# Kernel optimization log

Measured on AMD Instinct MI355X. Metric: run time of the kernel, lower is better.

Reference implementation:

```python
import jax, jax.numpy as jnp
import numpy as np

N_ENT = 100000
N_USR = 1024
E = 400000
D = 128
H = 4
R = 32


def setup_inputs() -> dict:
    key = jax.random.key(0)
    ks = jax.random.split(key, 9)
    a = float(np.sqrt(6.0 / (D + D)))  # xavier_uniform bound for [D, D]
    return {
        "entity_emb": jax.random.normal(ks[0], (N_ENT, D), dtype=jnp.float32),
        "user_emb": jax.random.normal(ks[1], (N_USR, D), dtype=jnp.float32),
        "interact_mat": jnp.zeros((1,), dtype=jnp.float32),  # unused by forward
        "weight": jax.random.normal(ks[2], (R, D), dtype=jnp.float32) * 0.1,
        "qTrans": jax.random.uniform(ks[3], (D, D), minval=-a, maxval=a, dtype=jnp.float32),
        "kTrans": jax.random.uniform(ks[4], (D, D), minval=-a, maxval=a, dtype=jnp.float32),
        "vTrans": jax.random.uniform(ks[5], (D, D), minval=-a, maxval=a, dtype=jnp.float32),
        "edge_index": jax.random.randint(ks[6], (2, E), 0, N_ENT, dtype=jnp.int64)
            if jax.config.jax_enable_x64 else jax.random.randint(ks[6], (2, E), 0, N_ENT, dtype=jnp.int32),
        "edge_type": jax.random.randint(ks[7], (E,), 1, R + 1, dtype=jnp.int32),  # types in [1, R]
        "layer": 0,
    }


def _kglayer(rows, col_embeds, embeds, n_seg, qT, kT, vT):
    # rows: [E] target-node index, col_embeds: [E, D] edge messages
    dh = D // H
    row_embeds = embeds[rows]                              # gather [E, D]
    q = (row_embeds @ qT).reshape(-1, H, dh)
    k = (col_embeds @ kT).reshape(-1, H, dh)
    v = (col_embeds @ vT).reshape(-1, H, dh)
    att = jnp.clip(jnp.einsum("ehd,ehd->eh", q, k), -10.0, 10.0)
    exp_att = jnp.exp(att)                                 # [E, H]
    att_norm = jax.ops.segment_sum(exp_att, rows, num_segments=n_seg)[rows]
    att = exp_att / (att_norm + 1e-8)
    res = (att[..., None] * v).reshape(-1, D)              # [E, D]
    return jax.ops.segment_sum(res, rows, num_segments=n_seg)


def _sim_hrt(head_emb, tail_emb, rel_emb):
    # per-edge scalar attention logit [E, 1]
    tr = jnp.linalg.norm(tail_emb * rel_emb, axis=1, keepdims=True)
    hr = jnp.linalg.norm(head_emb * rel_emb, axis=1, keepdims=True)
    return (hr * tr) ** 2


def reference(entity_emb, user_emb, interact_mat, weight, qTrans, kTrans, vTrans,
              edge_index, edge_type, layer):
    n_entities = entity_emb.shape[0]
    head, tail = edge_index[0], edge_index[1]
    rel = weight[edge_type - 1]                            # [E, D]
    neigh = entity_emb[tail] * rel                         # [E, D]
    kg_emb = _kglayer(head, neigh, entity_emb, n_entities, qTrans, kTrans, vTrans)
    w = _sim_hrt(kg_emb[head], kg_emb[tail], rel)          # [E, 1]
    w = jnp.broadcast_to(w, neigh.shape)                   # expand to [E, D]
    # scatter_softmax over edges sharing the same head (numerically stable)
    m = jax.ops.segment_max(w, head, num_segments=n_entities)[head]
    e = jnp.exp(w - m)
    s = jax.ops.segment_sum(e, head, num_segments=n_entities)[head]
    soft = e / s
    msg = soft * entity_emb[tail]
    return jax.ops.segment_sum(msg, head, num_segments=n_entities)
```

## Files before the change

kernel.cpp:

```cpp
#include <hip/hip_runtime.h>
#include <cstdint>

#define D 128
#define H 4
#define N_ENT 100000
#define N_EDGE 400000
#define R 32

#define SCAN_NB ((N_ENT + 511) / 512)

__global__ void k_hist(const int* __restrict__ head, int* __restrict__ deg) {
  const int e = blockIdx.x * 256 + threadIdx.x;
  if (e < N_EDGE) atomicAdd(&deg[head[e]], 1);
}

__global__ __launch_bounds__(256) void k_scan1(const int* __restrict__ deg,
                                               int* __restrict__ bsum) {
  const int t = threadIdx.x;
  const int i = blockIdx.x * 512 + t * 2;
  int v0 = (i < N_ENT) ? deg[i] : 0;
  int v1 = (i + 1 < N_ENT) ? deg[i + 1] : 0;
  int s = v0 + v1;
#pragma unroll
  for (int k = 1; k < 64; k <<= 1) s += __shfl_xor(s, k);
  __shared__ int ws[4];
  if ((t & 63) == 0) ws[t >> 6] = s;
  __syncthreads();
  if (t == 0) bsum[blockIdx.x] = ws[0] + ws[1] + ws[2] + ws[3];
}

__global__ __launch_bounds__(256) void k_scan2(const int* __restrict__ bsum,
                                               int* __restrict__ bbase,
                                               int* __restrict__ off) {
  __shared__ int sh[256];
  const int t = threadIdx.x;
  const int v = (t < SCAN_NB) ? bsum[t] : 0;
  sh[t] = v;
  __syncthreads();
  for (int d = 1; d < 256; d <<= 1) {
    const int u = (t >= d) ? sh[t - d] : 0;
    __syncthreads();
    sh[t] += u;
    __syncthreads();
  }
  if (t < SCAN_NB) bbase[t] = sh[t] - v;
  if (t == SCAN_NB - 1) off[N_ENT] = sh[t];
}

__global__ __launch_bounds__(256) void k_scan3(const int* __restrict__ deg,
                                               const int* __restrict__ bbase,
                                               int* __restrict__ off,
                                               int* __restrict__ cur) {
  __shared__ int sh[256];
  const int t = threadIdx.x;
  const int i = blockIdx.x * 512 + t * 2;
  const int v0 = (i < N_ENT) ? deg[i] : 0;
  const int v1 = (i + 1 < N_ENT) ? deg[i + 1] : 0;
  const int s = v0 + v1;
  sh[t] = s;
  __syncthreads();
  for (int d = 1; d < 256; d <<= 1) {
    const int u = (t >= d) ? sh[t - d] : 0;
    __syncthreads();
    sh[t] += u;
    __syncthreads();
  }
  const int ex = sh[t] - s + bbase[blockIdx.x];
  if (i < N_ENT) {
    off[i] = ex;
    cur[i] = ex;
  }
  if (i + 1 < N_ENT) {
    off[i + 1] = ex + v0;
    cur[i + 1] = ex + v0;
  }
}

__global__ void k_scatter(const int* __restrict__ head,
                          const int* __restrict__ tail,
                          const int* __restrict__ etype, int* __restrict__ cur,
                          int* __restrict__ tailP, int* __restrict__ etypeP) {
  const int e = blockIdx.x * 256 + threadIdx.x;
  if (e >= N_EDGE) return;
  const int hd = head[e];
  const int pos = atomicAdd(&cur[hd], 1);
  tailP[pos] = tail[e];
  etypeP[pos] = etype[e] - 1;
}

__global__ __launch_bounds__(256) void k_tr(const float* __restrict__ in,
                                            float* __restrict__ out) {
  __shared__ float tile[32][33];
  const int bx = blockIdx.x & 3, by = blockIdx.x >> 2;
  const int c = threadIdx.x & 31;
  const int r0 = (threadIdx.x >> 5) * 4;
#pragma unroll
  for (int i = 0; i < 4; ++i)
    tile[r0 + i][c] = in[(by * 32 + r0 + i) * 128 + bx * 32 + c];
  __syncthreads();
#pragma unroll
  for (int i = 0; i < 4; ++i)
    out[(bx * 32 + r0 + i) * 128 + by * 32 + c] = tile[c][r0 + i];
}

__global__ __launch_bounds__(512) void k_qproj(const float* __restrict__ ent,
                                               const float* __restrict__ qT,
                                               float* __restrict__ Q) {
  __shared__ float sT[D * D];
  __shared__ float rows[D * 128];
  const int t = threadIdx.x;
  const int n0 = blockIdx.x * 128;
#pragma unroll
  for (int s = 0; s < 8; ++s) {
    const int idx = (s * 512 + t) * 4;
    *(float4*)&sT[idx] = *(const float4*)&qT[idx];
  }
  {
    const int g = t & 3;
    const int n = t >> 2;
    const int node = n0 + n;
    if (node < N_ENT) {
      const float* src = ent + (size_t)node * D;
#pragma unroll
      for (int s = 0; s < 8; ++s) {
        const int i = s * 16 + g * 4;
        float4 v = *(const float4*)&src[i];
        rows[(i + 0) * 128 + n] = v.x;
        rows[(i + 1) * 128 + n] = v.y;
        rows[(i + 2) * 128 + n] = v.z;
        rows[(i + 3) * 128 + n] = v.w;
      }
    } else {
#pragma unroll
      for (int s = 0; s < 8; ++s) {
        const int i = s * 16 + g * 4;
        rows[(i + 0) * 128 + n] = 0.f;
        rows[(i + 1) * 128 + n] = 0.f;
        rows[(i + 2) * 128 + n] = 0.f;
        rows[(i + 3) * 128 + n] = 0.f;
      }
    }
  }
  __syncthreads();
  const int jj = t & 15;
  const int ee = t >> 4;
  float acc[4][8];
#pragma unroll
  for (int a = 0; a < 4; ++a)
#pragma unroll
    for (int b = 0; b < 8; ++b) acc[a][b] = 0.f;
#pragma unroll 4
  for (int i = 0; i < D; ++i) {
    float4 b0 = *(float4*)&sT[i * D + jj * 8];
    float4 b1 = *(float4*)&sT[i * D + jj * 8 + 4];
    float4 a0 = *(float4*)&rows[i * 128 + ee * 4];
    float bv[8] = {b0.x, b0.y, b0.z, b0.w, b1.x, b1.y, b1.z, b1.w};
    float av[4] = {a0.x, a0.y, a0.z, a0.w};
#pragma unroll
    for (int a = 0; a < 4; ++a)
#pragma unroll
      for (int b = 0; b < 8; ++b) acc[a][b] = fmaf(av[a], bv[b], acc[a][b]);
  }
#pragma unroll
  for (int a = 0; a < 4; ++a) {
    const int node = n0 + ee * 4 + a;
    if (node < N_ENT) {
      float4 o0 = {acc[a][0], acc[a][1], acc[a][2], acc[a][3]};
      float4 o1 = {acc[a][4], acc[a][5], acc[a][6], acc[a][7]};
      *(float4*)&Q[(size_t)node * D + jj * 8] = o0;
      *(float4*)&Q[(size_t)node * D + jj * 8 + 4] = o1;
    }
  }
}

__global__ __launch_bounds__(256, 4) void k_fused(
    const float* __restrict__ ent, const float* __restrict__ wrel,
    const float* __restrict__ kTt, const float* __restrict__ vT, float* qkg,
    const int* __restrict__ off, const int* __restrict__ tailP,
    const int* __restrict__ etypeP) {
  __shared__ float sQ[8 * 128];
  __shared__ float sP[8 * 512];
  __shared__ float sAgg[8 * 512];
  const int t = threadIdx.x;
  const int base = blockIdx.x * 8;

  {
    const int k = t >> 5;
    const int c4 = (t & 31) * 4;
    *(float4*)&sQ[k * 128 + c4] =
        *(const float4*)&qkg[(size_t)(base + k) * D + c4];
  }
  __syncthreads();

  {
    const int i = t & 127;
    const int sub = t >> 7;
    float pp[2][8];
#pragma unroll
    for (int hh = 0; hh < 2; ++hh)
#pragma unroll
      for (int k = 0; k < 8; ++k) pp[hh][k] = 0.f;
#pragma unroll
    for (int hh = 0; hh < 2; ++hh) {
      const int h = sub * 2 + hh;
      for (int c = 0; c < 32; ++c) {
        const float kv = kTt[(h * 32 + c) * 128 + i];
#pragma unroll
        for (int k = 0; k < 8; ++k)
          pp[hh][k] = fmaf(kv, sQ[k * 128 + h * 32 + c], pp[hh][k]);
      }
    }
#pragma unroll
    for (int hh = 0; hh < 2; ++hh)
#pragma unroll
      for (int k = 0; k < 8; ++k)
        sP[k * 512 + (sub * 2 + hh) * 128 + i] = pp[hh][k];
  }
  __syncthreads();

  {
    const int wid = t >> 6;
    const int half = (t >> 5) & 1;
    const int l32 = t & 31;
    const int k = wid * 2 + half;
    const int n = base + k;
    const float4 P0 = *(const float4*)&sP[k * 512 + 0 * 128 + l32 * 4];
    const float4 P1 = *(const float4*)&sP[k * 512 + 1 * 128 + l32 * 4];
    const float4 P2 = *(const float4*)&sP[k * 512 + 2 * 128 + l32 * 4];
    const float4 P3 = *(const float4*)&sP[k * 512 + 3 * 128 + l32 * 4];
    float4 a0 = {0, 0, 0, 0}, a1 = {0, 0, 0, 0};
    float4 a2 = {0, 0, 0, 0}, a3 = {0, 0, 0, 0};
    float s0 = 0.f, s1 = 0.f, s2 = 0.f, s3 = 0.f;
    const int eb = off[n];
    const int deg = off[n + 1] - eb;
    for (int idx = 0; idx < deg; ++idx) {
      const int e = eb + idx;
      const int tl = tailP[e];
      const int ty = etypeP[e];
      const float4 x = *(const float4*)&ent[(size_t)tl * D + l32 * 4];
      const float4 r = *(const float4*)&wrel[(size_t)ty * D + l32 * 4];
      const float4 nh = {x.x * r.x, x.y * r.y, x.z * r.z, x.w * r.w};
      float d0 = nh.x * P0.x + nh.y * P0.y + nh.z * P0.z + nh.w * P0.w;
      float d1 = nh.x * P1.x + nh.y * P1.y + nh.z * P1.z + nh.w * P1.w;
      float d2 = nh.x * P2.x + nh.y * P2.y + nh.z * P2.z + nh.w * P2.w;
      float d3 = nh.x * P3.x + nh.y * P3.y + nh.z * P3.z + nh.w * P3.w;
#pragma unroll
      for (int s = 1; s < 32; s <<= 1) {
        d0 += __shfl_xor(d0, s);
        d1 += __shfl_xor(d1, s);
        d2 += __shfl_xor(d2, s);
        d3 += __shfl_xor(d3, s);
      }
      const float e0 = expf(fminf(fmaxf(d0, -10.f), 10.f));
      const float e1 = expf(fminf(fmaxf(d1, -10.f), 10.f));
      const float e2 = expf(fminf(fmaxf(d2, -10.f), 10.f));
      const float e3 = expf(fminf(fmaxf(d3, -10.f), 10.f));
      a0.x = fmaf(e0, nh.x, a0.x); a0.y = fmaf(e0, nh.y, a0.y);
      a0.z = fmaf(e0, nh.z, a0.z); a0.w = fmaf(e0, nh.w, a0.w);
      a1.x = fmaf(e1, nh.x, a1.x); a1.y = fmaf(e1, nh.y, a1.y);
      a1.z = fmaf(e1, nh.z, a1.z); a1.w = fmaf(e1, nh.w, a1.w);
      a2.x = fmaf(e2, nh.x, a2.x); a2.y = fmaf(e2, nh.y, a2.y);
      a2.z = fmaf(e2, nh.z, a2.z); a2.w = fmaf(e2, nh.w, a2.w);
      a3.x = fmaf(e3, nh.x, a3.x); a3.y = fmaf(e3, nh.y, a3.y);
      a3.z = fmaf(e3, nh.z, a3.z); a3.w = fmaf(e3, nh.w, a3.w);
      s0 += e0; s1 += e1; s2 += e2; s3 += e3;
    }
    const float i0 = 1.f / (s0 + 1e-8f);
    const float i1 = 1.f / (s1 + 1e-8f);
    const float i2 = 1.f / (s2 + 1e-8f);
    const float i3 = 1.f / (s3 + 1e-8f);
    float4 o0 = {a0.x * i0, a0.y * i0, a0.z * i0, a0.w * i0};
    float4 o1 = {a1.x * i1, a1.y * i1, a1.z * i1, a1.w * i1};
    float4 o2 = {a2.x * i2, a2.y * i2, a2.z * i2, a2.w * i2};
    float4 o3 = {a3.x * i3, a3.y * i3, a3.z * i3, a3.w * i3};
    *(float4*)&sAgg[k * 512 + 0 * 128 + l32 * 4] = o0;
    *(float4*)&sAgg[k * 512 + 1 * 128 + l32 * 4] = o1;
    *(float4*)&sAgg[k * 512 + 2 * 128 + l32 * 4] = o2;
    *(float4*)&sAgg[k * 512 + 3 * 128 + l32 * 4] = o3;
  }
  __syncthreads();

  {
    const int c = t & 127;
    const int g4 = (t >> 7) * 4;
    const int h = c >> 5;
    float acc0 = 0.f, acc1 = 0.f, acc2 = 0.f, acc3 = 0.f;
    const float* agg0 = &sAgg[(g4 + 0) * 512 + h * 128];
    const float* agg1 = &sAgg[(g4 + 1) * 512 + h * 128];
    const float* agg2 = &sAgg[(g4 + 2) * 512 + h * 128];
    const float* agg3 = &sAgg[(g4 + 3) * 512 + h * 128];
#pragma unroll 4
    for (int d = 0; d < 128; ++d) {
      const float v = vT[d * 128 + c];
      acc0 = fmaf(agg0[d], v, acc0);
      acc1 = fmaf(agg1[d], v, acc1);
      acc2 = fmaf(agg2[d], v, acc2);
      acc3 = fmaf(agg3[d], v, acc3);
    }
    qkg[(size_t)(base + g4 + 0) * D + c] = acc0;
    qkg[(size_t)(base + g4 + 1) * D + c] = acc1;
    qkg[(size_t)(base + g4 + 2) * D + c] = acc2;
    qkg[(size_t)(base + g4 + 3) * D + c] = acc3;
  }
}

__global__ __launch_bounds__(256) void k_S(const float* __restrict__ kg,
                                           const float* __restrict__ wrel,
                                           float* __restrict__ S) {
  __shared__ float sB[D * 32];
  __shared__ float sA[D * 64];
  const int t = threadIdx.x;
  const int n0 = blockIdx.x * 64;
  {
    const int r = t & 31;
    const int qg = t >> 5;
#pragma unroll
    for (int s = 0; s < 4; ++s) {
      const int d = qg * 16 + s * 4;
      float4 b = *(const float4*)&wrel[(size_t)r * D + d];
      sB[(d + 0) * 32 + r] = b.x * b.x;
      sB[(d + 1) * 32 + r] = b.y * b.y;
      sB[(d + 2) * 32 + r] = b.z * b.z;
      sB[(d + 3) * 32 + r] = b.w * b.w;
    }
  }
  {
    const int nn = t & 63;
    const int dg = t >> 6;
    const int node = n0 + nn;
#pragma unroll
    for (int s = 0; s < 8; ++s) {
      const int d = dg * 32 + s * 4;
      float4 a = {0, 0, 0, 0};
      if (node < N_ENT) a = *(const float4*)&kg[(size_t)node * D + d];
      sA[(d + 0) * 64 + nn] = a.x * a.x;
      sA[(d + 1) * 64 + nn] = a.y * a.y;
      sA[(d + 2) * 64 + nn] = a.z * a.z;
      sA[(d + 3) * 64 + nn] = a.w * a.w;
    }
  }
  __syncthreads();
  const int nn2 = t >> 2;
  const int rg = t & 3;
  float acc[8];
#pragma unroll
  for (int c = 0; c < 8; ++c) acc[c] = 0.f;
#pragma unroll 4
  for (int d = 0; d < D; ++d) {
    const float a = sA[d * 64 + nn2];
    float4 b0 = *(float4*)&sB[d * 32 + rg * 8];
    float4 b1 = *(float4*)&sB[d * 32 + rg * 8 + 4];
    acc[0] = fmaf(a, b0.x, acc[0]);
    acc[1] = fmaf(a, b0.y, acc[1]);
    acc[2] = fmaf(a, b0.z, acc[2]);
    acc[3] = fmaf(a, b0.w, acc[3]);
    acc[4] = fmaf(a, b1.x, acc[4]);
    acc[5] = fmaf(a, b1.y, acc[5]);
    acc[6] = fmaf(a, b1.z, acc[6]);
    acc[7] = fmaf(a, b1.w, acc[7]);
  }
  const int node = n0 + nn2;
  if (node < N_ENT) {
    float4 o0 = {acc[0], acc[1], acc[2], acc[3]};
    float4 o1 = {acc[4], acc[5], acc[6], acc[7]};
    *(float4*)&S[(size_t)node * 32 + rg * 8] = o0;
    *(float4*)&S[(size_t)node * 32 + rg * 8 + 4] = o1;
  }
}

__global__ __launch_bounds__(256) void k_out2(
    const float* __restrict__ ent, const float* __restrict__ S,
    const int* __restrict__ off, const int* __restrict__ tailP,
    const int* __restrict__ etypeP, float* __restrict__ out) {
  const int t = threadIdx.x;
  const int wid = t >> 6;
  const int lane = t & 63;
  const int n = blockIdx.x * 4 + wid;
  if (n >= N_ENT) return;
  const int eb = off[n];
  const int deg = off[n + 1] - eb;
  float accx = 0.f, accy = 0.f;
  float m = 0.f, ssum = 0.f;
  for (int b = 0; b < deg; b += 64) {
    const int idx = b + lane;
    const bool val = idx < deg;
    const int e = eb + (val ? idx : 0);
    const int tl = tailP[e];
    const int ty = etypeP[e];
    float w = val ? S[(size_t)n * 32 + ty] * S[(size_t)tl * 32 + ty] : -1.f;
    float cm = w;
#pragma unroll
    for (int k = 1; k < 64; k <<= 1) cm = fmaxf(cm, __shfl_xor(cm, k));
    const float mnew = fmaxf(m, cm);
    const float scale = expf(m - mnew);
    const float el = val ? expf(w - mnew) : 0.f;
    float cs = el;
#pragma unroll
    for (int k = 1; k < 64; k <<= 1) cs += __shfl_xor(cs, k);
    ssum = ssum * scale + cs;
    accx *= scale;
    accy *= scale;
    const int cnt = (deg - b < 64) ? deg - b : 64;
    for (int j = 0; j < cnt; ++j) {
      const float sj = __shfl(el, j);
      const int tlj = __shfl(tl, j);
      const float2 x = *(const float2*)&ent[(size_t)tlj * D + lane * 2];
      accx = fmaf(sj, x.x, accx);
      accy = fmaf(sj, x.y, accy);
    }
    m = mnew;
  }
  const float inv = (deg > 0) ? 1.f / ssum : 0.f;
  float2 o = {accx * inv, accy * inv};
  *(float2*)&out[(size_t)n * D + lane * 2] = o;
}

extern "C" void kernel_launch(void* const* d_in, const int* in_sizes, int n_in,
                              void* d_out, int out_size, void* d_ws,
                              size_t ws_size, hipStream_t stream) {
  const float* ent = (const float*)d_in[0];
  const float* wrel = (const float*)d_in[3];
  const float* qT = (const float*)d_in[4];
  const float* kT = (const float*)d_in[5];
  const float* vT = (const float*)d_in[6];
  const int* eidx = (const int*)d_in[7];
  const int* etype = (const int*)d_in[8];
  const int* head = eidx;
  const int* tail = eidx + N_EDGE;

  float* S = (float*)d_ws;
  int* off = (int*)(S + (size_t)N_ENT * 32);
  int* cur = off + (N_ENT + 1);
  int* deg = cur + N_ENT;
  int* bsum = deg + N_ENT;
  int* bbase = bsum + SCAN_NB;
  int* tailP = bbase + SCAN_NB;
  int* etypeP = tailP + N_EDGE;
  float* kTt = (float*)(etypeP + N_EDGE);
  float* qkg = (float*)d_out;

  hipMemsetAsync(deg, 0, N_ENT * sizeof(int), stream);
  k_hist<<<(N_EDGE + 255) / 256, 256, 0, stream>>>(head, deg);
  k_scan1<<<SCAN_NB, 256, 0, stream>>>(deg, bsum);
  k_scan2<<<1, 256, 0, stream>>>(bsum, bbase, off);
  k_scan3<<<SCAN_NB, 256, 0, stream>>>(deg, bbase, off, cur);
  k_scatter<<<(N_EDGE + 255) / 256, 256, 0, stream>>>(head, tail, etype, cur,
                                                      tailP, etypeP);
  k_tr<<<16, 256, 0, stream>>>(kT, kTt);
  k_qproj<<<(N_ENT + 127) / 128, 512, 0, stream>>>(ent, qT, qkg);
  k_fused<<<N_ENT / 8, 256, 0, stream>>>(ent, wrel, kTt, vT, qkg, off, tailP,
                                         etypeP);
  k_S<<<(N_ENT + 63) / 64, 256, 0, stream>>>(qkg, wrel, S);
  k_out2<<<(N_ENT + 3) / 4, 256, 0, stream>>>(ent, S, off, tailP, etypeP,
                                              qkg);
}
```

Measured before the change: 561.0 us.

## Split fused attention kernel into tiled P-projection, edge, and V-projection kernels

```diff
diff --git a/kernel.cpp b/kernel.cpp
--- a/kernel.cpp
+++ b/kernel.cpp
@@ -8,6 +8,7 @@
 #define R 32
 
 #define SCAN_NB ((N_ENT + 511) / 512)
+#define CDIV(a, b) (((a) + (b) - 1) / (b))
 
 __global__ void k_hist(const int* __restrict__ head, int* __restrict__ deg) {
   const int e = blockIdx.x * 256 + threadIdx.x;
@@ -88,21 +89,6 @@
   etypeP[pos] = etype[e] - 1;
 }
 
-__global__ __launch_bounds__(256) void k_tr(const float* __restrict__ in,
-                                            float* __restrict__ out) {
-  __shared__ float tile[32][33];
-  const int bx = blockIdx.x & 3, by = blockIdx.x >> 2;
-  const int c = threadIdx.x & 31;
-  const int r0 = (threadIdx.x >> 5) * 4;
-#pragma unroll
-  for (int i = 0; i < 4; ++i)
-    tile[r0 + i][c] = in[(by * 32 + r0 + i) * 128 + bx * 32 + c];
-  __syncthreads();
-#pragma unroll
-  for (int i = 0; i < 4; ++i)
-    out[(bx * 32 + r0 + i) * 128 + by * 32 + c] = tile[c][r0 + i];
-}
-
 __global__ __launch_bounds__(512) void k_qproj(const float* __restrict__ ent,
                                                const float* __restrict__ qT,
                                                float* __restrict__ Q) {
@@ -173,134 +159,220 @@
   }
 }
 
-__global__ __launch_bounds__(256, 4) void k_fused(
-    const float* __restrict__ ent, const float* __restrict__ wrel,
-    const float* __restrict__ kTt, const float* __restrict__ vT, float* qkg,
-    const int* __restrict__ off, const int* __restrict__ tailP,
-    const int* __restrict__ etypeP) {
-  __shared__ float sQ[8 * 128];
-  __shared__ float sP[8 * 512];
-  __shared__ float sAgg[8 * 512];
-  const int t = threadIdx.x;
-  const int base = blockIdx.x * 8;
-
-  {
-    const int k = t >> 5;
-    const int c4 = (t & 31) * 4;
-    *(float4*)&sQ[k * 128 + c4] =
-        *(const float4*)&qkg[(size_t)(base + k) * D + c4];
-  }
-  __syncthreads();
-
+__global__ __launch_bounds__(256) void k_pproj(const float* __restrict__ Q,
+                                               const float* __restrict__ kT,
+                                               float* __restrict__ pbuf,
+                                               const int c0, const int cn) {
+  __shared__ float sB[32 * 128];
+  __shared__ float sA[32 * 128];
+  const int t = threadIdx.x;
+  const int h = blockIdx.y;
+  const int n0 = blockIdx.x * 128;
   {
     const int i = t & 127;
-    const int sub = t >> 7;
-    float pp[2][8];
-#pragma unroll
-    for (int hh = 0; hh < 2; ++hh)
-#pragma unroll
-      for (int k = 0; k < 8; ++k) pp[hh][k] = 0.f;
-#pragma unroll
-    for (int hh = 0; hh < 2; ++hh) {
-      const int h = sub * 2 + hh;
-      for (int c = 0; c < 32; ++c) {
-        const float kv = kTt[(h * 32 + c) * 128 + i];
-#pragma unroll
-        for (int k = 0; k < 8; ++k)
-          pp[hh][k] = fmaf(kv, sQ[k * 128 + h * 32 + c], pp[hh][k]);
+    const int jh = t >> 7;
+    const float* kr = kT + (size_t)i * D + h * 32 + jh * 16;
+#pragma unroll
+    for (int s = 0; s < 4; ++s) {
+      float4 v = *(const float4*)&kr[s * 4];
+      const int j = jh * 16 + s * 4;
+      sB[(j + 0) * 128 + i] = v.x;
+      sB[(j + 1) * 128 + i] = v.y;
+      sB[(j + 2) * 128 + i] = v.z;
+      sB[(j + 3) * 128 + i] = v.w;
+    }
+  }
+  {
+    const int nn = t & 127;
+    const int jh = t >> 7;
+    float4 v[4] = {{0, 0, 0, 0}, {0, 0, 0, 0}, {0, 0, 0, 0}, {0, 0, 0, 0}};
+    if (n0 + nn < cn) {
+      const float* qr = Q + (size_t)(c0 + n0 + nn) * D + h * 32 + jh * 16;
+#pragma unroll
+      for (int s = 0; s < 4; ++s) v[s] = *(const float4*)&qr[s * 4];
+    }
+#pragma unroll
+    for (int s = 0; s < 4; ++s) {
+      const int j = jh * 16 + s * 4;
+      sA[(j + 0) * 128 + nn] = v[s].x;
+      sA[(j + 1) * 128 + nn] = v[s].y;
+      sA[(j + 2) * 128 + nn] = v[s].z;
+      sA[(j + 3) * 128 + nn] = v[s].w;
+    }
+  }
+  __syncthreads();
+  const int ng = t & 15;
+  const int ig = t >> 4;
+  float acc[8][8];
+#pragma unroll
+  for (int a = 0; a < 8; ++a)
+#pragma unroll
+    for (int b = 0; b < 8; ++b) acc[a][b] = 0.f;
+#pragma unroll 4
+  for (int j = 0; j < 32; ++j) {
+    float4 a0 = *(float4*)&sA[j * 128 + ng * 8];
+    float4 a1 = *(float4*)&sA[j * 128 + ng * 8 + 4];
+    float4 b0 = *(float4*)&sB[j * 128 + ig * 8];
+    float4 b1 = *(float4*)&sB[j * 128 + ig * 8 + 4];
+    float av[8] = {a0.x, a0.y, a0.z, a0.w, a1.x, a1.y, a1.z, a1.w};
+    float bv[8] = {b0.x, b0.y, b0.z, b0.w, b1.x, b1.y, b1.z, b1.w};
+#pragma unroll
+    for (int a = 0; a < 8; ++a)
+#pragma unroll
+      for (int b = 0; b < 8; ++b) acc[a][b] = fmaf(av[a], bv[b], acc[a][b]);
+  }
+#pragma unroll
+  for (int a = 0; a < 8; ++a) {
+    const int ln = n0 + ng * 8 + a;
+    if (ln < cn) {
+      float4 o0 = {acc[a][0], acc[a][1], acc[a][2], acc[a][3]};
+      float4 o1 = {acc[a][4], acc[a][5], acc[a][6], acc[a][7]};
+      *(float4*)&pbuf[(size_t)ln * 512 + h * 128 + ig * 8] = o0;
+      *(float4*)&pbuf[(size_t)ln * 512 + h * 128 + ig * 8 + 4] = o1;
+    }
+  }
+}
+
+__global__ __launch_bounds__(256) void k_edge(
+    const float* __restrict__ ent, const float* __restrict__ wrel,
+    float* __restrict__ pbuf, const int* __restrict__ off,
+    const int* __restrict__ tailP, const int* __restrict__ etypeP,
+    const int c0, const int cn) {
+  const int t = threadIdx.x;
+  const int l32 = t & 31;
+  const int ln = blockIdx.x * 8 + (t >> 5);
+  if (ln >= cn) return;
+  const int n = c0 + ln;
+  float* prow = pbuf + (size_t)ln * 512 + l32 * 4;
+  const float4 P0 = *(const float4*)&prow[0];
+  const float4 P1 = *(const float4*)&prow[128];
+  const float4 P2 = *(const float4*)&prow[256];
+  const float4 P3 = *(const float4*)&prow[384];
+  float4 a0 = {0, 0, 0, 0}, a1 = {0, 0, 0, 0};
+  float4 a2 = {0, 0, 0, 0}, a3 = {0, 0, 0, 0};
+  float s0 = 0.f, s1 = 0.f, s2 = 0.f, s3 = 0.f;
+  const int eb = off[n];
+  const int deg = off[n + 1] - eb;
+  for (int idx = 0; idx < deg; ++idx) {
+    const int e = eb + idx;
+    const int tl = tailP[e];
+    const int ty = etypeP[e];
+    const float4 x = *(const float4*)&ent[(size_t)tl * D + l32 * 4];
+    const float4 r = *(const float4*)&wrel[(size_t)ty * D + l32 * 4];
+    const float4 nh = {x.x * r.x, x.y * r.y, x.z * r.z, x.w * r.w};
+    float d0 = nh.x * P0.x + nh.y * P0.y + nh.z * P0.z + nh.w * P0.w;
+    float d1 = nh.x * P1.x + nh.y * P1.y + nh.z * P1.z + nh.w * P1.w;
+    float d2 = nh.x * P2.x + nh.y * P2.y + nh.z * P2.z + nh.w * P2.w;
+    float d3 = nh.x * P3.x + nh.y * P3.y + nh.z * P3.z + nh.w * P3.w;
+    float a01 = (l32 & 1) ? d1 : d0;
+    float b01 = (l32 & 1) ? d0 : d1;
+    a01 += __shfl_xor(b01, 1);
+    float a23 = (l32 & 1) ? d3 : d2;
+    float b23 = (l32 & 1) ? d2 : d3;
+    a23 += __shfl_xor(b23, 1);
+    float A = (l32 & 2) ? a23 : a01;
+    float B = (l32 & 2) ? a01 : a23;
+    A += __shfl_xor(B, 2);
+    A += __shfl_xor(A, 4);
+    A += __shfl_xor(A, 8);
+    A += __shfl_xor(A, 16);
+    const float ew = expf(fminf(fmaxf(A, -10.f), 10.f));
+    const float e0 = __shfl(ew, 0, 4);
+    const float e1 = __shfl(ew, 1, 4);
+    const float e2 = __shfl(ew, 2, 4);
+    const float e3 = __shfl(ew, 3, 4);
+    a0.x = fmaf(e0, nh.x, a0.x); a0.y = fmaf(e0, nh.y, a0.y);
+    a0.z = fmaf(e0, nh.z, a0.z); a0.w = fmaf(e0, nh.w, a0.w);
+    a1.x = fmaf(e1, nh.x, a1.x); a1.y = fmaf(e1, nh.y, a1.y);
+    a1.z = fmaf(e1, nh.z, a1.z); a1.w = fmaf(e1, nh.w, a1.w);
+    a2.x = fmaf(e2, nh.x, a2.x); a2.y = fmaf(e2, nh.y, a2.y);
+    a2.z = fmaf(e2, nh.z, a2.z); a2.w = fmaf(e2, nh.w, a2.w);
+    a3.x = fmaf(e3, nh.x, a3.x); a3.y = fmaf(e3, nh.y, a3.y);
+    a3.z = fmaf(e3, nh.z, a3.z); a3.w = fmaf(e3, nh.w, a3.w);
+    s0 += e0; s1 += e1; s2 += e2; s3 += e3;
+  }
+  const float i0 = 1.f / (s0 + 1e-8f);
+  const float i1 = 1.f / (s1 + 1e-8f);
+  const float i2 = 1.f / (s2 + 1e-8f);
+  const float i3 = 1.f / (s3 + 1e-8f);
+  float4 o0 = {a0.x * i0, a0.y * i0, a0.z * i0, a0.w * i0};
+  float4 o1 = {a1.x * i1, a1.y * i1, a1.z * i1, a1.w * i1};
+  float4 o2 = {a2.x * i2, a2.y * i2, a2.z * i2, a2.w * i2};
+  float4 o3 = {a3.x * i3, a3.y * i3, a3.z * i3, a3.w * i3};
+  *(float4*)&prow[0] = o0;
+  *(float4*)&prow[128] = o1;
+  *(float4*)&prow[256] = o2;
+  *(float4*)&prow[384] = o3;
+}
+
+__global__ __launch_bounds__(128) void k_kg(const float* __restrict__ agg,
+                                            const float* __restrict__ vT,
+                                            float* __restrict__ kg,
+                                            const int c0, const int cn) {
+  __shared__ float sA[32 * 256];
+  __shared__ float sB[32 * 32];
+  const int t = threadIdx.x;
+  const int h = blockIdx.y;
+  const int n0 = blockIdx.x * 256;
+  const int ng = t & 31;
+  const int cg = t >> 5;
+  float acc[8][8];
+#pragma unroll
+  for (int a = 0; a < 8; ++a)
+#pragma unroll
+    for (int b = 0; b < 8; ++b) acc[a][b] = 0.f;
+  for (int kc = 0; kc < 4; ++kc) {
+    {
+      const int jj = t >> 2;
+      const int cq = (t & 3) * 8;
+      const float* vr = vT + (size_t)(kc * 32 + jj) * D + h * 32 + cq;
+      *(float4*)&sB[jj * 32 + cq] = *(const float4*)&vr[0];
+      *(float4*)&sB[jj * 32 + cq + 4] = *(const float4*)&vr[4];
+    }
+#pragma unroll
+    for (int u = 0; u < 2; ++u) {
+      const int nn = t * 2 + u;
+      float4 v[8] = {{0, 0, 0, 0}, {0, 0, 0, 0}, {0, 0, 0, 0}, {0, 0, 0, 0},
+                     {0, 0, 0, 0}, {0, 0, 0, 0}, {0, 0, 0, 0}, {0, 0, 0, 0}};
+      if (n0 + nn < cn) {
+        const float* ar = agg + (size_t)(n0 + nn) * 512 + h * 128 + kc * 32;
+#pragma unroll
+        for (int s = 0; s < 8; ++s) v[s] = *(const float4*)&ar[s * 4];
       }
-    }
-#pragma unroll
-    for (int hh = 0; hh < 2; ++hh)
-#pragma unroll
-      for (int k = 0; k < 8; ++k)
-        sP[k * 512 + (sub * 2 + hh) * 128 + i] = pp[hh][k];
-  }
-  __syncthreads();
-
-  {
-    const int wid = t >> 6;
-    const int half = (t >> 5) & 1;
-    const int l32 = t & 31;
-    const int k = wid * 2 + half;
-    const int n = base + k;
-    const float4 P0 = *(const float4*)&sP[k * 512 + 0 * 128 + l32 * 4];
-    const float4 P1 = *(const float4*)&sP[k * 512 + 1 * 128 + l32 * 4];
-    const float4 P2 = *(const float4*)&sP[k * 512 + 2 * 128 + l32 * 4];
-    const float4 P3 = *(const float4*)&sP[k * 512 + 3 * 128 + l32 * 4];
-    float4 a0 = {0, 0, 0, 0}, a1 = {0, 0, 0, 0};
-    float4 a2 = {0, 0, 0, 0}, a3 = {0, 0, 0, 0};
-    float s0 = 0.f, s1 = 0.f, s2 = 0.f, s3 = 0.f;
-    const int eb = off[n];
-    const int deg = off[n + 1] - eb;
-    for (int idx = 0; idx < deg; ++idx) {
-      const int e = eb + idx;
-      const int tl = tailP[e];
-      const int ty = etypeP[e];
-      const float4 x = *(const float4*)&ent[(size_t)tl * D + l32 * 4];
-      const float4 r = *(const float4*)&wrel[(size_t)ty * D + l32 * 4];
-      const float4 nh = {x.x * r.x, x.y * r.y, x.z * r.z, x.w * r.w};
-      float d0 = nh.x * P0.x + nh.y * P0.y + nh.z * P0.z + nh.w * P0.w;
-      float d1 = nh.x * P1.x + nh.y * P1.y + nh.z * P1.z + nh.w * P1.w;
-      float d2 = nh.x * P2.x + nh.y * P2.y + nh.z * P2.z + nh.w * P2.w;
-      float d3 = nh.x * P3.x + nh.y * P3.y + nh.z * P3.z + nh.w * P3.w;
-#pragma unroll
-      for (int s = 1; s < 32; s <<= 1) {
-        d0 += __shfl_xor(d0, s);
-        d1 += __shfl_xor(d1, s);
-        d2 += __shfl_xor(d2, s);
-        d3 += __shfl_xor(d3, s);
+#pragma unroll
+      for (int s = 0; s < 8; ++s) {
+        const int j = s * 4;
+        sA[(j + 0) * 256 + nn] = v[s].x;
+        sA[(j + 1) * 256 + nn] = v[s].y;
+        sA[(j + 2) * 256 + nn] = v[s].z;
+        sA[(j + 3) * 256 + nn] = v[s].w;
       }
-      const float e0 = expf(fminf(fmaxf(d0, -10.f), 10.f));
-      const float e1 = expf(fminf(fmaxf(d1, -10.f), 10.f));
-      const float e2 = expf(fminf(fmaxf(d2, -10.f), 10.f));
-      const float e3 = expf(fminf(fmaxf(d3, -10.f), 10.f));
-      a0.x = fmaf(e0, nh.x, a0.x); a0.y = fmaf(e0, nh.y, a0.y);
-      a0.z = fmaf(e0, nh.z, a0.z); a0.w = fmaf(e0, nh.w, a0.w);
-      a1.x = fmaf(e1, nh.x, a1.x); a1.y = fmaf(e1, nh.y, a1.y);
-      a1.z = fmaf(e1, nh.z, a1.z); a1.w = fmaf(e1, nh.w, a1.w);
-      a2.x = fmaf(e2, nh.x, a2.x); a2.y = fmaf(e2, nh.y, a2.y);
-      a2.z = fmaf(e2, nh.z, a2.z); a2.w = fmaf(e2, nh.w, a2.w);
-      a3.x = fmaf(e3, nh.x, a3.x); a3.y = fmaf(e3, nh.y, a3.y);
-      a3.z = fmaf(e3, nh.z, a3.z); a3.w = fmaf(e3, nh.w, a3.w);
-      s0 += e0; s1 += e1; s2 += e2; s3 += e3;
-    }
-    const float i0 = 1.f / (s0 + 1e-8f);
-    const float i1 = 1.f / (s1 + 1e-8f);
-    const float i2 = 1.f / (s2 + 1e-8f);
-    const float i3 = 1.f / (s3 + 1e-8f);
-    float4 o0 = {a0.x * i0, a0.y * i0, a0.z * i0, a0.w * i0};
-    float4 o1 = {a1.x * i1, a1.y * i1, a1.z * i1, a1.w * i1};
-    float4 o2 = {a2.x * i2, a2.y * i2, a2.z * i2, a2.w * i2};
-    float4 o3 = {a3.x * i3, a3.y * i3, a3.z * i3, a3.w * i3};
-    *(float4*)&sAgg[k * 512 + 0 * 128 + l32 * 4] = o0;
-    *(float4*)&sAgg[k * 512 + 1 * 128 + l32 * 4] = o1;
-    *(float4*)&sAgg[k * 512 + 2 * 128 + l32 * 4] = o2;
-    *(float4*)&sAgg[k * 512 + 3 * 128 + l32 * 4] = o3;
-  }
-  __syncthreads();
-
-  {
-    const int c = t & 127;
-    const int g4 = (t >> 7) * 4;
-    const int h = c >> 5;
-    float acc0 = 0.f, acc1 = 0.f, acc2 = 0.f, acc3 = 0.f;
-    const float* agg0 = &sAgg[(g4 + 0) * 512 + h * 128];
-    const float* agg1 = &sAgg[(g4 + 1) * 512 + h * 128];
-    const float* agg2 = &sAgg[(g4 + 2) * 512 + h * 128];
-    const float* agg3 = &sAgg[(g4 + 3) * 512 + h * 128];
+    }
+    __syncthreads();
 #pragma unroll 4
-    for (int d = 0; d < 128; ++d) {
-      const float v = vT[d * 128 + c];
-      acc0 = fmaf(agg0[d], v, acc0);
-      acc1 = fmaf(agg1[d], v, acc1);
-      acc2 = fmaf(agg2[d], v, acc2);
-      acc3 = fmaf(agg3[d], v, acc3);
-    }
-    qkg[(size_t)(base + g4 + 0) * D + c] = acc0;
-    qkg[(size_t)(base + g4 + 1) * D + c] = acc1;
-    qkg[(size_t)(base + g4 + 2) * D + c] = acc2;
-    qkg[(size_t)(base + g4 + 3) * D + c] = acc3;
+    for (int j = 0; j < 32; ++j) {
+      float4 a0 = *(float4*)&sA[j * 256 + ng * 8];
+      float4 a1 = *(float4*)&sA[j * 256 + ng * 8 + 4];
+      float4 b0 = *(float4*)&sB[j * 32 + cg * 8];
+      float4 b1 = *(float4*)&sB[j * 32 + cg * 8 + 4];
+      float av[8] = {a0.x, a0.y, a0.z, a0.w, a1.x, a1.y, a1.z, a1.w};
+      float bv[8] = {b0.x, b0.y, b0.z, b0.w, b1.x, b1.y, b1.z, b1.w};
+#pragma unroll
+      for (int a = 0; a < 8; ++a)
+#pragma unroll
+        for (int b = 0; b < 8; ++b) acc[a][b] = fmaf(av[a], bv[b], acc[a][b]);
+    }
+    __syncthreads();
+  }
+#pragma unroll
+  for (int a = 0; a < 8; ++a) {
+    const int ln = n0 + ng * 8 + a;
+    if (ln < cn) {
+      float4 o0 = {acc[a][0], acc[a][1], acc[a][2], acc[a][3]};
+      float4 o1 = {acc[a][4], acc[a][5], acc[a][6], acc[a][7]};
+      *(float4*)&kg[(size_t)(c0 + ln) * D + h * 32 + cg * 8] = o0;
+      *(float4*)&kg[(size_t)(c0 + ln) * D + h * 32 + cg * 8 + 4] = o1;
+    }
   }
 }
 
@@ -436,7 +508,14 @@
   int* bbase = bsum + SCAN_NB;
   int* tailP = bbase + SCAN_NB;
   int* etypeP = tailP + N_EDGE;
-  float* kTt = (float*)(etypeP + N_EDGE);
+  size_t fixedBytes = (size_t)((char*)(etypeP + N_EDGE) - (char*)d_ws);
+  fixedBytes = (fixedBytes + 255) & ~(size_t)255;
+  float* pbuf = (float*)((char*)d_ws + fixedBytes);
+  size_t avail = (ws_size > fixedBytes) ? ws_size - fixedBytes : 0;
+  long long cap = (long long)(avail / (512 * sizeof(float)));
+  if (cap > N_ENT) cap = N_ENT;
+  cap &= ~7LL;
+  if (cap < 8) cap = 8;
   float* qkg = (float*)d_out;
 
   hipMemsetAsync(deg, 0, N_ENT * sizeof(int), stream);
@@ -446,10 +525,16 @@
   k_scan3<<<SCAN_NB, 256, 0, stream>>>(deg, bbase, off, cur);
   k_scatter<<<(N_EDGE + 255) / 256, 256, 0, stream>>>(head, tail, etype, cur,
                                                       tailP, etypeP);
-  k_tr<<<16, 256, 0, stream>>>(kT, kTt);
   k_qproj<<<(N_ENT + 127) / 128, 512, 0, stream>>>(ent, qT, qkg);
-  k_fused<<<N_ENT / 8, 256, 0, stream>>>(ent, wrel, kTt, vT, qkg, off, tailP,
-                                         etypeP);
+  for (int c0 = 0; c0 < N_ENT; c0 += (int)cap) {
+    const int cn = (N_ENT - c0 < (int)cap) ? (N_ENT - c0) : (int)cap;
+    dim3 gp(CDIV(cn, 128), H);
+    k_pproj<<<gp, 256, 0, stream>>>(qkg, kT, pbuf, c0, cn);
+    k_edge<<<CDIV(cn, 8), 256, 0, stream>>>(ent, wrel, pbuf, off, tailP,
+                                            etypeP, c0, cn);
+    dim3 gk(CDIV(cn, 256), H);
+    k_kg<<<gk, 128, 0, stream>>>(pbuf, vT, qkg, c0, cn);
+  }
   k_S<<<(N_ENT + 63) / 64, 256, 0, stream>>>(qkg, wrel, S);
   k_out2<<<(N_ENT + 3) / 4, 256, 0, stream>>>(ent, S, off, tailP, etypeP,
                                               qkg);
```

Result: slower. 573.7 us (+2.3%).
